# Kernel optimization log

Measured on AMD Instinct MI355X. Metric: run time of the kernel, lower is better.

## Reference

```python
import jax, jax.numpy as jnp
import numpy as np

B_, N_, E_, NNZ = 64, 1723, 1723, 16384
CIN, COUT = 256, 256
H1, H2, H3 = 64, 32, 128  # lin1 out, HGCN hidden, HGCN out (hidden_channels=128)


def layernorm(x, g, b, eps=1e-5):
    mu = jnp.mean(x, axis=-1, keepdims=True)
    var = jnp.mean((x - mu) ** 2, axis=-1, keepdims=True)
    return (x - mu) * jax.lax.rsqrt(var + eps) * g + b


def graph_linear(x, W, b):
    # x: (B, Cin, N) -> (B, Cout, N), matches torch.matmul(W[None], x) + b[None,:,None]
    return jnp.einsum('oc,bcn->bon', W, x) + b[None, :, None]


def hconv(x, node_idx, edge_idx, theta, bias):
    # PyG HypergraphConv (no attention): X' = D^-1 H W B^-1 H^T X Theta + bias
    x = jnp.einsum('bnc,oc->bno', x, theta)  # lin (bias=False)
    ones = jnp.ones(node_idx.shape, x.dtype)
    Dd = jax.ops.segment_sum(ones, node_idx, num_segments=N_)  # node degree
    Bd = jax.ops.segment_sum(ones, edge_idx, num_segments=E_)  # hyperedge degree
    Dinv = jnp.where(Dd > 0, 1.0 / Dd, 0.0)
    Binv = jnp.where(Bd > 0, 1.0 / Bd, 0.0)
    # node -> hyperedge aggregation, message scaled by B^-1 of target edge
    msg = jnp.swapaxes(x[:, node_idx, :] * Binv[edge_idx][None, :, None], 0, 1)  # (nnz,B,C)
    ef = jax.ops.segment_sum(msg, edge_idx, num_segments=E_)  # (E,B,C)
    # hyperedge -> node aggregation, message scaled by D^-1 of target node
    msg2 = ef[edge_idx] * Dinv[node_idx][:, None, None]  # (nnz,B,C)
    out = jax.ops.segment_sum(msg2, node_idx, num_segments=N_)  # (N,B,C)
    return jnp.swapaxes(out, 0, 1) + bias


def setup_inputs():
    key = jax.random.key(0)
    ks = jax.random.split(key, 8)
    s = 0.02
    return {
        'x': jax.random.normal(ks[0], (B_, N_, CIN), jnp.float32),
        'incident_matrix': jax.random.randint(ks[1], (2, NNZ), 0, N_, jnp.int32),
        'pre_g': jnp.ones((CIN,), jnp.float32),
        'pre_b': jnp.zeros((CIN,), jnp.float32),
        'lin1_W': jax.random.normal(ks[2], (H1, CIN), jnp.float32) * s,
        'lin1_b': jnp.zeros((H1,), jnp.float32),
        'n1_g': jnp.ones((H1,), jnp.float32),
        'n1_b': jnp.zeros((H1,), jnp.float32),
        'th1': jax.random.normal(ks[3], (H2, H1), jnp.float32) * s,
        'bi1': jnp.zeros((H2,), jnp.float32),
        'th2': jax.random.normal(ks[4], (H3, H2), jnp.float32) * s,
        'bi2': jnp.zeros((H3,), jnp.float32),
        'n2_g': jnp.ones((H3,), jnp.float32),
        'n2_b': jnp.zeros((H3,), jnp.float32),
        'lin2_W': jax.random.normal(ks[5], (COUT, H3), jnp.float32) * s,
        'lin2_b': jnp.zeros((COUT,), jnp.float32),
    }


def reference(x, incident_matrix, pre_g, pre_b, lin1_W, lin1_b, n1_g, n1_b,
              th1, bi1, th2, bi2, n2_g, n2_b, lin2_W, lin2_b):
    node_idx, edge_idx = incident_matrix[0], incident_matrix[1]
    ty = jnp.swapaxes(jax.nn.relu(layernorm(x, pre_g, pre_b)), 1, 2)  # (B,Cin,N)
    y = jnp.swapaxes(graph_linear(ty, lin1_W, lin1_b), 1, 2)          # (B,N,64)
    y = jax.nn.relu(layernorm(y, n1_g, n1_b))
    y = hconv(y, node_idx, edge_idx, th1, bi1)                         # (B,N,32)
    y = hconv(y, node_idx, edge_idx, th2, bi2)                         # (B,N,128)
    ty = jnp.swapaxes(jax.nn.relu(layernorm(y, n2_g, n2_b)), 1, 2)
    y = jnp.swapaxes(graph_linear(ty, lin2_W, lin2_b), 1, 2)           # (B,N,256)
    return x + y  # skip_conv declared in module but unused in forward
```

## Files before the change

kernel.cpp:

```cpp
#include <hip/hip_runtime.h>
#include <cstdint>

constexpr int B  = 64;
constexpr int N  = 1723;
constexpr int E  = 1723;
constexpr int NNZ = 16384;
constexpr int ROWS = B * N;

typedef __bf16 bf16x8 __attribute__((ext_vector_type(8)));
typedef float  f32x4  __attribute__((ext_vector_type(4)));

constexpr size_t OFF_DD   = 0;
constexpr size_t OFF_BD   = OFF_DD + E;
constexpr size_t OFF_NCUR = OFF_BD + E;
constexpr size_t OFF_ECUR = OFF_NCUR + E;
constexpr size_t OFF_NOFF = OFF_ECUR + E;
constexpr size_t OFF_EOFF = OFF_NOFF + (E + 1);
constexpr size_t OFF_NVAL = OFF_EOFF + (E + 1);
constexpr size_t OFF_EVAL = OFF_NVAL + NNZ;

constexpr int WB_LIN1 = 0;
constexpr int WB_TH1  = 16384;
constexpr int WB_TH2  = 18432;
constexpr int WB_LIN2 = 22528;
constexpr int WB_TOT  = 55296;
constexpr int CVT_BLOCKS  = WB_TOT / 8 / 256;
constexpr int ZERO_INTS   = 4 * E;
constexpr int ZERO_BLOCKS = (ZERO_INTS + 255) / 256;

constexpr size_t B_WB    = 262144;
constexpr size_t B_SLOTA = 1u << 20;
constexpr size_t B_SLOTB = B_SLOTA + (30u << 20);
constexpr size_t B_SLOTC = B_SLOTB + (8u << 20);
constexpr size_t B_SLOTD = B_SLOTC + (8u << 20);

__device__ __forceinline__ ushort f2bf(float f) {
  uint32_t b = __float_as_uint(f);
  b += 0x7fffu + ((b >> 16) & 1u);
  return (ushort)(b >> 16);
}
__device__ __forceinline__ float bf2f(ushort u) {
  return __uint_as_float((uint32_t)u << 16);
}
union U16x8 { uint4 q; ushort s[8]; };

__global__ __launch_bounds__(256) void k_init(const float* __restrict__ W1, const float* __restrict__ W2,
                                              const float* __restrict__ W3, const float* __restrict__ W4,
                                              ushort* __restrict__ out, int* __restrict__ zr) {
  int bid = blockIdx.x;
  if (bid < CVT_BLOCKS) {
    int e = (bid * 256 + threadIdx.x) * 8;
    const float* src;
    int off;
    if (e < WB_TH1)      { src = W1; off = e - WB_LIN1; }
    else if (e < WB_TH2) { src = W2; off = e - WB_TH1; }
    else if (e < WB_LIN2){ src = W3; off = e - WB_TH2; }
    else                 { src = W4; off = e - WB_LIN2; }
    float4 v0 = *(const float4*)(src + off);
    float4 v1 = *(const float4*)(src + off + 4);
    U16x8 u;
    u.s[0] = f2bf(v0.x); u.s[1] = f2bf(v0.y); u.s[2] = f2bf(v0.z); u.s[3] = f2bf(v0.w);
    u.s[4] = f2bf(v1.x); u.s[5] = f2bf(v1.y); u.s[6] = f2bf(v1.z); u.s[7] = f2bf(v1.w);
    *(uint4*)(out + e) = u.q;
  } else {
    int i = (bid - CVT_BLOCKS) * 256 + threadIdx.x;
    if (i < ZERO_INTS) zr[i] = 0;
  }
}

__global__ __launch_bounds__(256) void k_hist(const int* __restrict__ inc,
                                              int* __restrict__ Dd, int* __restrict__ Bd) {
  int k = blockIdx.x * 256 + threadIdx.x;
  atomicAdd(&Dd[inc[k]], 1);
  atomicAdd(&Bd[inc[NNZ + k]], 1);
}

__global__ __launch_bounds__(256) void k_scan(const int* __restrict__ Dd, const int* __restrict__ Bd,
                                              int* __restrict__ noff, int* __restrict__ eoff) {
  __shared__ int part[256];
  const int t = threadIdx.x;
  for (int pass = 0; pass < 2; ++pass) {
    const int* cnt = pass ? Bd : Dd;
    int* off = pass ? eoff : noff;
    constexpr int CH = 7;
    int loc[CH];
    int s = 0;
    int base = t * CH;
#pragma unroll
    for (int i = 0; i < CH; ++i) {
      int idx = base + i;
      loc[i] = (idx < E) ? cnt[idx] : 0;
      s += loc[i];
    }
    part[t] = s;
    __syncthreads();
    for (int d = 1; d < 256; d <<= 1) {
      int v = (t >= d) ? part[t - d] : 0;
      __syncthreads();
      part[t] += v;
      __syncthreads();
    }
    int pre = (t > 0) ? part[t - 1] : 0;
#pragma unroll
    for (int i = 0; i < CH; ++i) {
      int idx = base + i;
      if (idx < E) off[idx] = pre;
      pre += loc[i];
    }
    if (t == 255) off[E] = pre;
    __syncthreads();
  }
}

__global__ __launch_bounds__(256) void k_fill(const int* __restrict__ inc,
                                              const int* __restrict__ noff, const int* __restrict__ eoff,
                                              int* __restrict__ ncur, int* __restrict__ ecur,
                                              int* __restrict__ nval, int* __restrict__ eval) {
  int k = blockIdx.x * 256 + threadIdx.x;
  int n = inc[k], e = inc[NNZ + k];
  int p = atomicAdd(&ecur[e], 1);
  eval[eoff[e] + p] = n;
  int q = atomicAdd(&ncur[n], 1);
  nval[noff[n] + q] = e;
}

__global__ __launch_bounds__(256) void k_sort2(const int* __restrict__ noff, int* __restrict__ nval,
                                               const int* __restrict__ eoff, int* __restrict__ eval) {
  __shared__ int buf[256][33];
  int s = blockIdx.x * 256 + threadIdx.x;
  const int* off;
  int* vals;
  if (s < E) { off = noff; vals = nval; }
  else if (s < 2 * E) { off = eoff; vals = eval; s -= E; }
  else return;
  int b = off[s], e = off[s + 1], len = e - b;
  int* loc = buf[threadIdx.x];
  if (len <= 32) {
    for (int i = 0; i < len; ++i) loc[i] = vals[b + i];
    for (int i = 1; i < len; ++i) {
      int v = loc[i];
      int j = i - 1;
      while (j >= 0 && loc[j] > v) { loc[j + 1] = loc[j]; --j; }
      loc[j + 1] = v;
    }
    for (int i = 0; i < len; ++i) vals[b + i] = loc[i];
  } else {
    for (int i = b + 1; i < e; ++i) {
      int v = vals[i];
      int j = i - 1;
      while (j >= b && vals[j] > v) { vals[j + 1] = vals[j]; --j; }
      vals[j + 1] = v;
    }
  }
}

__global__ __launch_bounds__(256, 3) void k_lin1th1(const float* __restrict__ x,
                                                    const ushort* __restrict__ Wb,
                                                    const float* __restrict__ lin1_b,
                                                    const float* __restrict__ pre_g,
                                                    const float* __restrict__ pre_b,
                                                    const float* __restrict__ n1_g,
                                                    const float* __restrict__ n1_b,
                                                    ushort* __restrict__ xl1) {
  __shared__ __align__(16) uint4 R0[2048];
  __shared__ __align__(16) uint4 W2s[256];
  __shared__ float2 st[64];

  const int t = threadIdx.x;
  const int r0 = blockIdx.x * 64;
  const ushort* W1 = Wb + WB_LIN1;
  const ushort* W2 = Wb + WB_TH1;

  const int lane = t & 63;
  const int w = t >> 6;
  const int lo = lane & 15, hi = lane >> 4;
  const int wm = w & 1, wn = w >> 1;
  const int m0 = wm * 32 + lo, m1 = wm * 32 + 16 + lo;

  bf16x8 wf[16];
#pragma unroll
  for (int ks = 0; ks < 8; ++ks)
#pragma unroll
    for (int f = 0; f < 2; ++f) {
      int n = wn * 32 + f * 16 + lo;
      wf[ks * 2 + f] = *(const bf16x8*)(W1 + (size_t)n * 256 + (ks * 4 + hi) * 8);
    }

  {
    int row = t >> 3, c = t & 7;
    W2s[row * 8 + (c ^ (row & 7))] = *(const uint4*)(W2 + row * 64 + c * 8);
  }
#pragma unroll
  for (int i = 0; i < 8; ++i) {
    int idx = t + i * 256;
    int row = idx >> 5, c = idx & 31;
    const float* src = x + (size_t)(r0 + row) * 256 + c * 8;
    float4 v0 = *(const float4*)src;
    float4 v1 = *(const float4*)(src + 4);
    U16x8 u;
    u.s[0] = f2bf(v0.x); u.s[1] = f2bf(v0.y); u.s[2] = f2bf(v0.z); u.s[3] = f2bf(v0.w);
    u.s[4] = f2bf(v1.x); u.s[5] = f2bf(v1.y); u.s[6] = f2bf(v1.z); u.s[7] = f2bf(v1.w);
    R0[row * 32 + (c ^ (row & 7))] = u.q;
  }
  __syncthreads();

  {
    int row = t >> 2, part = t & 3;
    float s1 = 0.f, s2 = 0.f;
#pragma unroll
    for (int i = 0; i < 8; ++i) {
      int c = part * 8 + i;
      U16x8 u; u.q = R0[row * 32 + (c ^ (row & 7))];
#pragma unroll
      for (int j = 0; j < 8; ++j) { float v = bf2f(u.s[j]); s1 += v; s2 += v * v; }
    }
    s1 += __shfl_xor(s1, 1, 64); s2 += __shfl_xor(s2, 1, 64);
    s1 += __shfl_xor(s1, 2, 64); s2 += __shfl_xor(s2, 2, 64);
    if (part == 0) {
      float mu = s1 / 256.f;
      float var = fmaxf(s2 / 256.f - mu * mu, 0.f);
      st[row] = make_float2(mu, rsqrtf(var + 1e-5f));
    }
  }
  __syncthreads();
#pragma unroll
  for (int i = 0; i < 8; ++i) {
    int idx = t + i * 256;
    int row = idx >> 5, c = idx & 31;
    int slot = row * 32 + (c ^ (row & 7));
    U16x8 u; u.q = R0[slot];
    float2 s = st[row];
    float4 g0 = *(const float4*)(pre_g + c * 8);
    float4 g1 = *(const float4*)(pre_g + c * 8 + 4);
    float4 b0 = *(const float4*)(pre_b + c * 8);
    float4 b1 = *(const float4*)(pre_b + c * 8 + 4);
    U16x8 o;
    o.s[0] = f2bf(fmaxf(fmaf((bf2f(u.s[0]) - s.x) * s.y, g0.x, b0.x), 0.f));
    o.s[1] = f2bf(fmaxf(fmaf((bf2f(u.s[1]) - s.x) * s.y, g0.y, b0.y), 0.f));
    o.s[2] = f2bf(fmaxf(fmaf((bf2f(u.s[2]) - s.x) * s.y, g0.z, b0.z), 0.f));
    o.s[3] = f2bf(fmaxf(fmaf((bf2f(u.s[3]) - s.x) * s.y, g0.w, b0.w), 0.f));
    o.s[4] = f2bf(fmaxf(fmaf((bf2f(u.s[4]) - s.x) * s.y, g1.x, b1.x), 0.f));
    o.s[5] = f2bf(fmaxf(fmaf((bf2f(u.s[5]) - s.x) * s.y, g1.y, b1.y), 0.f));
    o.s[6] = f2bf(fmaxf(fmaf((bf2f(u.s[6]) - s.x) * s.y, g1.z, b1.z), 0.f));
    o.s[7] = f2bf(fmaxf(fmaf((bf2f(u.s[7]) - s.x) * s.y, g1.w, b1.w), 0.f));
    R0[slot] = o.q;
  }
  __syncthreads();

  const bf16x8* Asv = (const bf16x8*)R0;
  f32x4 acc1[2][2] = {};
#pragma unroll
  for (int ks = 0; ks < 8; ++ks) {
    int cb = ks * 4 + hi;
    bf16x8 a0 = Asv[m0 * 32 + (cb ^ (m0 & 7))];
    bf16x8 a1 = Asv[m1 * 32 + (cb ^ (m1 & 7))];
#pragma unroll
    for (int f = 0; f < 2; ++f) {
      acc1[0][f] = __builtin_amdgcn_mfma_f32_16x16x32_bf16(a0, wf[ks * 2 + f], acc1[0][f], 0, 0, 0);
      acc1[1][f] = __builtin_amdgcn_mfma_f32_16x16x32_bf16(a1, wf[ks * 2 + f], acc1[1][f], 0, 0, 0);
    }
  }
  __syncthreads();

  float* ost = (float*)R0;
#pragma unroll
  for (int f = 0; f < 2; ++f) {
    int colg = wn * 32 + f * 16 + lo;
    float badd = lin1_b[colg];
#pragma unroll
    for (int i = 0; i < 2; ++i)
#pragma unroll
      for (int r = 0; r < 4; ++r) {
        int lr = wm * 32 + i * 16 + hi * 4 + r;
        ost[lr * 68 + colg] = acc1[i][f][r] + badd;
      }
  }
  __syncthreads();

  {
    int row = t >> 2, part = t & 3;
    float s1 = 0.f, s2 = 0.f;
#pragma unroll
    for (int i = 0; i < 16; ++i) {
      float v = ost[row * 68 + part * 16 + i];
      s1 += v; s2 += v * v;
    }
    s1 += __shfl_xor(s1, 1, 64); s2 += __shfl_xor(s2, 1, 64);
    s1 += __shfl_xor(s1, 2, 64); s2 += __shfl_xor(s2, 2, 64);
    if (part == 0) {
      float mu = s1 / 64.f;
      float var = fmaxf(s2 / 64.f - mu * mu, 0.f);
      st[row] = make_float2(mu, rsqrtf(var + 1e-5f));
    }
  }
  __syncthreads();
  uint4* A2q = R0 + 1152;
#pragma unroll
  for (int i = 0; i < 2; ++i) {
    int idx = t + i * 256;
    int row = idx >> 3, c = idx & 7;
    float2 s = st[row];
    U16x8 u;
#pragma unroll
    for (int j = 0; j < 8; ++j) {
      int col = c * 8 + j;
      float v = ost[row * 68 + col];
      u.s[j] = f2bf(fmaxf(fmaf((v - s.x) * s.y, n1_g[col], n1_b[col]), 0.f));
    }
    A2q[row * 8 + (c ^ (row & 7))] = u.q;
  }
  __syncthreads();

  const bf16x8* A2v = (const bf16x8*)A2q;
  f32x4 acc2[2] = {};
#pragma unroll
  for (int ks = 0; ks < 2; ++ks) {
    int cb = ks * 4 + hi;
    bf16x8 a0 = A2v[m0 * 8 + (cb ^ (m0 & 7))];
    bf16x8 a1 = A2v[m1 * 8 + (cb ^ (m1 & 7))];
    int n = wn * 16 + lo;
    bf16x8 bfr = ((const bf16x8*)W2s)[n * 8 + (cb ^ (n & 7))];
    acc2[0] = __builtin_amdgcn_mfma_f32_16x16x32_bf16(a0, bfr, acc2[0], 0, 0, 0);
    acc2[1] = __builtin_amdgcn_mfma_f32_16x16x32_bf16(a1, bfr, acc2[1], 0, 0, 0);
  }
  {
    int colg = wn * 16 + lo;
#pragma unroll
    for (int i = 0; i < 2; ++i)
#pragma unroll
      for (int r = 0; r < 4; ++r) {
        int lr = wm * 32 + i * 16 + hi * 4 + r;
        ost[lr * 36 + colg] = acc2[i][r];
      }
  }
  __syncthreads();
  {
    int lr = t >> 2, c8 = t & 3;
    uint32_t r = r0 + lr;
    uint32_t b_ = r / (uint32_t)N;
    uint32_t n_ = r - b_ * (uint32_t)N;
    U16x8 u;
#pragma unroll
    for (int j = 0; j < 8; ++j) u.s[j] = f2bf(ost[lr * 36 + c8 * 8 + j]);
    *(uint4*)(xl1 + ((size_t)n_ * 64 + b_) * 32 + c8 * 8) = u.q;
  }
}

template <bool HASB>
__global__ __launch_bounds__(256) void agg_bf16_k(const ushort* __restrict__ in,
                                                  const int* __restrict__ off,
                                                  const int* __restrict__ vals,
                                                  const float* __restrict__ bias,
                                                  ushort* __restrict__ outb) {
  const int seg = blockIdx.x;
  const int beg = off[seg], end = off[seg + 1];
  const int t = threadIdx.x;
  float acc[8] = {0.f, 0.f, 0.f, 0.f, 0.f, 0.f, 0.f, 0.f};
  if (beg < end) {
    uint4 cur = *(const uint4*)(in + (size_t)vals[beg] * 2048 + t * 8);
    for (int k = beg + 1; k < end; ++k) {
      uint4 nxt = *(const uint4*)(in + (size_t)vals[k] * 2048 + t * 8);
      U16x8 u; u.q = cur;
#pragma unroll
      for (int j = 0; j < 8; ++j) acc[j] += bf2f(u.s[j]);
      cur = nxt;
    }
    U16x8 u; u.q = cur;
#pragma unroll
    for (int j = 0; j < 8; ++j) acc[j] += bf2f(u.s[j]);
  }
  float inv = (end > beg) ? 1.f / (float)(end - beg) : 0.f;
  U16x8 o;
  if constexpr (HASB) {
    int cb = (t & 3) * 8;
#pragma unroll
    for (int j = 0; j < 8; ++j) o.s[j] = f2bf(acc[j] * inv + bias[cb + j]);
  } else {
#pragma unroll
    for (int j = 0; j < 8; ++j) o.s[j] = f2bf(acc[j] * inv);
  }
  *(uint4*)(outb + (size_t)seg * 2048 + t * 8) = o.q;
}

__global__ __launch_bounds__(256, 2) void k_aggth2(const ushort* __restrict__ ef2,
                                                   const int* __restrict__ noff,
                                                   const int* __restrict__ nval,
                                                   const ushort* __restrict__ W2b,
                                                   const float* __restrict__ bi2,
                                                   const float* __restrict__ n2_g,
                                                   const float* __restrict__ n2_b,
                                                   ushort* __restrict__ y3n) {
  __shared__ __align__(16) uint4 A2s[256];
  __shared__ __align__(16) uint4 W2s[512];
  __shared__ float ost[64 * 132];
  __shared__ float2 st[64];
  const int t = threadIdx.x;
  const int seg = blockIdx.x;

#pragma unroll
  for (int i = 0; i < 2; ++i) {
    int idx = t + i * 256;
    int row = idx >> 2, c = idx & 3;
    W2s[row * 4 + (c ^ (row & 3))] = *(const uint4*)(W2b + row * 32 + c * 8);
  }
  const int beg = noff[seg], end = noff[seg + 1];
  float acc[8] = {0.f, 0.f, 0.f, 0.f, 0.f, 0.f, 0.f, 0.f};
  if (beg < end) {
    uint4 cur = *(const uint4*)(ef2 + (size_t)nval[beg] * 2048 + t * 8);
    for (int k = beg + 1; k < end; ++k) {
      uint4 nxt = *(const uint4*)(ef2 + (size_t)nval[k] * 2048 + t * 8);
      U16x8 u; u.q = cur;
#pragma unroll
      for (int j = 0; j < 8; ++j) acc[j] += bf2f(u.s[j]);
      cur = nxt;
    }
    U16x8 u; u.q = cur;
#pragma unroll
    for (int j = 0; j < 8; ++j) acc[j] += bf2f(u.s[j]);
  }
  float inv = (end > beg) ? 1.f / (float)(end - beg) : 0.f;
  {
    U16x8 u;
#pragma unroll
    for (int j = 0; j < 8; ++j) u.s[j] = f2bf(acc[j] * inv);
    int row = t >> 2, c = t & 3;
    A2s[row * 4 + (c ^ (row & 3))] = u.q;
  }
  __syncthreads();

  const int lane = t & 63;
  const int w = t >> 6;
  const int lo = lane & 15, hi = lane >> 4;
  const int wm = w & 1, wn = w >> 1;
  const int m0 = wm * 32 + lo, m1 = wm * 32 + 16 + lo;
  const bf16x8* Asv = (const bf16x8*)A2s;
  const bf16x8* Wsv = (const bf16x8*)W2s;
  f32x4 acc2[2][4] = {};
  {
    bf16x8 a0 = Asv[m0 * 4 + (hi ^ (m0 & 3))];
    bf16x8 a1 = Asv[m1 * 4 + (hi ^ (m1 & 3))];
#pragma unroll
    for (int f = 0; f < 4; ++f) {
      int n = wn * 64 + f * 16 + lo;
      bf16x8 bfr = Wsv[n * 4 + (hi ^ (n & 3))];
      acc2[0][f] = __builtin_amdgcn_mfma_f32_16x16x32_bf16(a0, bfr, acc2[0][f], 0, 0, 0);
      acc2[1][f] = __builtin_amdgcn_mfma_f32_16x16x32_bf16(a1, bfr, acc2[1][f], 0, 0, 0);
    }
  }
#pragma unroll
  for (int f = 0; f < 4; ++f) {
    int colg = wn * 64 + f * 16 + lo;
    float badd = bi2[colg];
#pragma unroll
    for (int i = 0; i < 2; ++i)
#pragma unroll
      for (int r = 0; r < 4; ++r) {
        int lr = wm * 32 + i * 16 + hi * 4 + r;
        ost[lr * 132 + colg] = acc2[i][f][r] + badd;
      }
  }
  __syncthreads();
  {
    int row = t >> 2, part = t & 3;
    float s1 = 0.f, s2 = 0.f;
#pragma unroll
    for (int i = 0; i < 32; ++i) {
      float v = ost[row * 132 + part * 32 + i];
      s1 += v; s2 += v * v;
    }
    s1 += __shfl_xor(s1, 1, 64); s2 += __shfl_xor(s2, 1, 64);
    s1 += __shfl_xor(s1, 2, 64); s2 += __shfl_xor(s2, 2, 64);
    if (part == 0) {
      float mu = s1 / 128.f;
      float var = fmaxf(s2 / 128.f - mu * mu, 0.f);
      st[row] = make_float2(mu, rsqrtf(var + 1e-5f));
    }
  }
  __syncthreads();
#pragma unroll
  for (int i = 0; i < 4; ++i) {
    int idx = t + i * 256;
    int row = idx >> 4, c = idx & 15;
    float2 s = st[row];
    U16x8 u;
#pragma unroll
    for (int j = 0; j < 8; ++j) {
      int col = c * 8 + j;
      float v = ost[row * 132 + col];
      u.s[j] = f2bf(fmaxf(fmaf((v - s.x) * s.y, n2_g[col], n2_b[col]), 0.f));
    }
    *(uint4*)(y3n + ((size_t)seg * 64 + row) * 128 + c * 8) = u.q;
  }
}

constexpr int NWG2 = (ROWS / 64) * 4;
__global__ __launch_bounds__(256, 2) void k_lin2(const ushort* __restrict__ y3n,
                                                 const ushort* __restrict__ Wl2,
                                                 const float* __restrict__ lin2_b,
                                                 const float* __restrict__ x,
                                                 float* __restrict__ out) {
  __shared__ __align__(16) uint4 smem[2048];
  const int t = threadIdx.x;
  int orig = blockIdx.x;
  int xcd = orig & 7;
  int idx0 = orig >> 3;
  constexpr int q = NWG2 / 8, r = NWG2 % 8;
  int wgid = (xcd < r ? xcd * (q + 1) : r * (q + 1) + (xcd - r) * q) + idx0;
  const int tile = wgid & 3;
  const int r0 = (wgid >> 2) * 64;
  const int c0 = tile * 64;
  uint4* AsQ = smem;
  uint4* WsQ = smem + 1024;

#pragma unroll
  for (int i = 0; i < 4; ++i) {
    int idx = t + i * 256;
    int row = idx >> 4, c = idx & 15;
    AsQ[row * 16 + (c ^ (row & 7))] = *(const uint4*)(y3n + (size_t)(r0 + row) * 128 + c * 8);
  }
#pragma unroll
  for (int i = 0; i < 4; ++i) {
    int idx = t + i * 256;
    int row = idx >> 4, c = idx & 15;
    WsQ[row * 16 + (c ^ (row & 7))] = *(const uint4*)(Wl2 + (size_t)(c0 + row) * 128 + c * 8);
  }
  __syncthreads();

  const int lane = t & 63;
  const int w = t >> 6;
  const int lo = lane & 15, hi = lane >> 4;
  const int wm = w & 1, wn = w >> 1;
  const int m0 = wm * 32 + lo, m1 = wm * 32 + 16 + lo;
  const bf16x8* Asv = (const bf16x8*)AsQ;
  const bf16x8* Wsv = (const bf16x8*)WsQ;
  f32x4 acc[2][2] = {};
#pragma unroll
  for (int ks = 0; ks < 4; ++ks) {
    int cb = ks * 4 + hi;
    bf16x8 a0 = Asv[m0 * 16 + (cb ^ (m0 & 7))];
    bf16x8 a1 = Asv[m1 * 16 + (cb ^ (m1 & 7))];
#pragma unroll
    for (int f = 0; f < 2; ++f) {
      int n = wn * 32 + f * 16 + lo;
      bf16x8 bfr = Wsv[n * 16 + (cb ^ (n & 7))];
      acc[0][f] = __builtin_amdgcn_mfma_f32_16x16x32_bf16(a0, bfr, acc[0][f], 0, 0, 0);
      acc[1][f] = __builtin_amdgcn_mfma_f32_16x16x32_bf16(a1, bfr, acc[1][f], 0, 0, 0);
    }
  }
  __syncthreads();

  float* ost = (float*)smem;
#pragma unroll
  for (int f = 0; f < 2; ++f) {
    int cl = wn * 32 + f * 16 + lo;
    float badd = lin2_b[c0 + cl];
#pragma unroll
    for (int i = 0; i < 2; ++i)
#pragma unroll
      for (int r2 = 0; r2 < 4; ++r2) {
        int lr = wm * 32 + i * 16 + hi * 4 + r2;
        ost[lr * 68 + cl] = acc[i][f][r2] + badd;
      }
  }
  __syncthreads();

#pragma unroll
  for (int i = 0; i < 4; ++i) {
    int idx = t + i * 256;
    int lr = idx >> 4, c4 = idx & 15;
    uint32_t rr = r0 + lr;
    uint32_t n_ = rr >> 6, b_ = rr & 63u;
    size_t obase = ((size_t)b_ * N + n_) * 256 + c0 + c4 * 4;
    float4 v = *(const float4*)&ost[lr * 68 + c4 * 4];
    float4 s = *(const float4*)(x + obase);
    v.x += s.x; v.y += s.y; v.z += s.z; v.w += s.w;
    *(float4*)(out + obase) = v;
  }
}

extern "C" void kernel_launch(void* const* d_in, const int* in_sizes, int n_in,
                              void* d_out, int out_size, void* d_ws, size_t ws_size,
                              hipStream_t stream) {
  const float* x      = (const float*)d_in[0];
  const int*   inc    = (const int*)  d_in[1];
  const float* pre_g  = (const float*)d_in[2];
  const float* pre_b  = (const float*)d_in[3];
  const float* lin1_W = (const float*)d_in[4];
  const float* lin1_b = (const float*)d_in[5];
  const float* n1_g   = (const float*)d_in[6];
  const float* n1_b   = (const float*)d_in[7];
  const float* th1    = (const float*)d_in[8];
  const float* bi1    = (const float*)d_in[9];
  const float* th2    = (const float*)d_in[10];
  const float* bi2    = (const float*)d_in[11];
  const float* n2_g   = (const float*)d_in[12];
  const float* n2_b   = (const float*)d_in[13];
  const float* lin2_W = (const float*)d_in[14];
  const float* lin2_b = (const float*)d_in[15];
  float* out = (float*)d_out;
  char* ws = (char*)d_ws;

  int* meta = (int*)ws;
  int* Dd   = meta + OFF_DD;
  int* Bd   = meta + OFF_BD;
  int* ncur = meta + OFF_NCUR;
  int* ecur = meta + OFF_ECUR;
  int* noff = meta + OFF_NOFF;
  int* eoff = meta + OFF_EOFF;
  int* nval = meta + OFF_NVAL;
  int* eval = meta + OFF_EVAL;

  ushort* Wbase = (ushort*)(ws + B_WB);
  ushort* y3n = (ushort*)(ws + B_SLOTA);
  ushort* xl1 = (ushort*)(ws + B_SLOTB);
  ushort* ef2 = (ushort*)(ws + B_SLOTB);
  ushort* ef1 = (ushort*)(ws + B_SLOTC);
  ushort* y2  = (ushort*)(ws + B_SLOTD);

  k_init<<<CVT_BLOCKS + ZERO_BLOCKS, 256, 0, stream>>>(lin1_W, th1, th2, lin2_W, Wbase, meta);

  k_hist<<<NNZ / 256, 256, 0, stream>>>(inc, Dd, Bd);
  k_scan<<<1, 256, 0, stream>>>(Dd, Bd, noff, eoff);
  k_fill<<<NNZ / 256, 256, 0, stream>>>(inc, noff, eoff, ncur, ecur, nval, eval);
  k_sort2<<<(2 * E + 255) / 256, 256, 0, stream>>>(noff, nval, eoff, eval);

  k_lin1th1<<<ROWS / 64, 256, 0, stream>>>(x, Wbase, lin1_b, pre_g, pre_b, n1_g, n1_b, xl1);

  agg_bf16_k<false><<<E, 256, 0, stream>>>(xl1, eoff, eval, nullptr, ef1);
  agg_bf16_k<true ><<<E, 256, 0, stream>>>(ef1, noff, nval, bi1, y2);
  agg_bf16_k<false><<<E, 256, 0, stream>>>(y2, eoff, eval, nullptr, ef2);

  k_aggth2<<<E, 256, 0, stream>>>(ef2, noff, nval, Wbase + WB_TH2, bi2, n2_g, n2_b, y3n);

  k_lin2<<<NWG2, 256, 0, stream>>>(y3n, Wbase + WB_LIN2, lin2_b, x, out);
}
```

Measured before the change: 165.9 us.

## Fuse final aggregation, theta2, layernorm with lin2 and residual into one kernel

Merges the k_aggth2 and k_lin2 kernels so that each node's 64x128 normalized activations stay in shared memory and feed the lin2 MFMA directly. The full lin2 weight (256x128) is loaded in two halves per block, and the output plus residual is written per node across the batch. This removes the y3n round trip through global memory and one launch. In exchange, each block re-reads the whole lin2 weight, uses more LDS (which may limit occupancy), and writes rows strided by N, giving less coalesced output.

```diff
diff --git a/kernel.cpp b/kernel.cpp
--- a/kernel.cpp
+++ b/kernel.cpp
@@ -29,8 +29,7 @@
 constexpr int ZERO_BLOCKS = (ZERO_INTS + 255) / 256;
 
 constexpr size_t B_WB    = 262144;
-constexpr size_t B_SLOTA = 1u << 20;
-constexpr size_t B_SLOTB = B_SLOTA + (30u << 20);
+constexpr size_t B_SLOTB = 4u << 20;
 constexpr size_t B_SLOTC = B_SLOTB + (8u << 20);
 constexpr size_t B_SLOTD = B_SLOTC + (8u << 20);
 
@@ -382,20 +381,30 @@
   *(uint4*)(outb + (size_t)seg * 2048 + t * 8) = o.q;
 }
 
-__global__ __launch_bounds__(256, 2) void k_aggth2(const ushort* __restrict__ ef2,
-                                                   const int* __restrict__ noff,
-                                                   const int* __restrict__ nval,
-                                                   const ushort* __restrict__ W2b,
-                                                   const float* __restrict__ bi2,
-                                                   const float* __restrict__ n2_g,
-                                                   const float* __restrict__ n2_b,
-                                                   ushort* __restrict__ y3n) {
+__global__ __launch_bounds__(256, 2) void k_aggl2(const ushort* __restrict__ ef2,
+                                                  const int* __restrict__ noff,
+                                                  const int* __restrict__ nval,
+                                                  const ushort* __restrict__ W2b,
+                                                  const float* __restrict__ bi2,
+                                                  const float* __restrict__ n2_g,
+                                                  const float* __restrict__ n2_b,
+                                                  const ushort* __restrict__ Wl2,
+                                                  const float* __restrict__ lin2_b,
+                                                  const float* __restrict__ x,
+                                                  float* __restrict__ out) {
   __shared__ __align__(16) uint4 A2s[256];
   __shared__ __align__(16) uint4 W2s[512];
-  __shared__ float ost[64 * 132];
+  __shared__ __align__(16) uint4 AsQ[1024];
+  __shared__ __align__(16) char  big[34816];
   __shared__ float2 st[64];
   const int t = threadIdx.x;
   const int seg = blockIdx.x;
+
+  const int lane = t & 63;
+  const int w = t >> 6;
+  const int lo = lane & 15, hi = lane >> 4;
+  const int wm = w & 1, wn = w >> 1;
+  const int m0 = wm * 32 + lo, m1 = wm * 32 + 16 + lo;
 
 #pragma unroll
   for (int i = 0; i < 2; ++i) {
@@ -428,15 +437,11 @@
   }
   __syncthreads();
 
-  const int lane = t & 63;
-  const int w = t >> 6;
-  const int lo = lane & 15, hi = lane >> 4;
-  const int wm = w & 1, wn = w >> 1;
-  const int m0 = wm * 32 + lo, m1 = wm * 32 + 16 + lo;
-  const bf16x8* Asv = (const bf16x8*)A2s;
-  const bf16x8* Wsv = (const bf16x8*)W2s;
-  f32x4 acc2[2][4] = {};
-  {
+  float* ost = (float*)big;
+  {
+    const bf16x8* Asv = (const bf16x8*)A2s;
+    const bf16x8* Wsv = (const bf16x8*)W2s;
+    f32x4 acc2[2][4] = {};
     bf16x8 a0 = Asv[m0 * 4 + (hi ^ (m0 & 3))];
     bf16x8 a1 = Asv[m1 * 4 + (hi ^ (m1 & 3))];
 #pragma unroll
@@ -446,18 +451,18 @@
       acc2[0][f] = __builtin_amdgcn_mfma_f32_16x16x32_bf16(a0, bfr, acc2[0][f], 0, 0, 0);
       acc2[1][f] = __builtin_amdgcn_mfma_f32_16x16x32_bf16(a1, bfr, acc2[1][f], 0, 0, 0);
     }
-  }
-#pragma unroll
-  for (int f = 0; f < 4; ++f) {
-    int colg = wn * 64 + f * 16 + lo;
-    float badd = bi2[colg];
-#pragma unroll
-    for (int i = 0; i < 2; ++i)
-#pragma unroll
-      for (int r = 0; r < 4; ++r) {
-        int lr = wm * 32 + i * 16 + hi * 4 + r;
-        ost[lr * 132 + colg] = acc2[i][f][r] + badd;
-      }
+#pragma unroll
+    for (int f = 0; f < 4; ++f) {
+      int colg = wn * 64 + f * 16 + lo;
+      float badd = bi2[colg];
+#pragma unroll
+      for (int i = 0; i < 2; ++i)
+#pragma unroll
+        for (int r = 0; r < 4; ++r) {
+          int lr = wm * 32 + i * 16 + hi * 4 + r;
+          ost[lr * 132 + colg] = acc2[i][f][r] + badd;
+        }
+    }
   }
   __syncthreads();
   {
@@ -489,92 +494,67 @@
       float v = ost[row * 132 + col];
       u.s[j] = f2bf(fmaxf(fmaf((v - s.x) * s.y, n2_g[col], n2_b[col]), 0.f));
     }
-    *(uint4*)(y3n + ((size_t)seg * 64 + row) * 128 + c * 8) = u.q;
-  }
-}
-
-constexpr int NWG2 = (ROWS / 64) * 4;
-__global__ __launch_bounds__(256, 2) void k_lin2(const ushort* __restrict__ y3n,
-                                                 const ushort* __restrict__ Wl2,
-                                                 const float* __restrict__ lin2_b,
-                                                 const float* __restrict__ x,
-                                                 float* __restrict__ out) {
-  __shared__ __align__(16) uint4 smem[2048];
-  const int t = threadIdx.x;
-  int orig = blockIdx.x;
-  int xcd = orig & 7;
-  int idx0 = orig >> 3;
-  constexpr int q = NWG2 / 8, r = NWG2 % 8;
-  int wgid = (xcd < r ? xcd * (q + 1) : r * (q + 1) + (xcd - r) * q) + idx0;
-  const int tile = wgid & 3;
-  const int r0 = (wgid >> 2) * 64;
-  const int c0 = tile * 64;
-  uint4* AsQ = smem;
-  uint4* WsQ = smem + 1024;
-
-#pragma unroll
-  for (int i = 0; i < 4; ++i) {
-    int idx = t + i * 256;
-    int row = idx >> 4, c = idx & 15;
-    AsQ[row * 16 + (c ^ (row & 7))] = *(const uint4*)(y3n + (size_t)(r0 + row) * 128 + c * 8);
-  }
-#pragma unroll
-  for (int i = 0; i < 4; ++i) {
-    int idx = t + i * 256;
-    int row = idx >> 4, c = idx & 15;
-    WsQ[row * 16 + (c ^ (row & 7))] = *(const uint4*)(Wl2 + (size_t)(c0 + row) * 128 + c * 8);
-  }
-  __syncthreads();
-
-  const int lane = t & 63;
-  const int w = t >> 6;
-  const int lo = lane & 15, hi = lane >> 4;
-  const int wm = w & 1, wn = w >> 1;
-  const int m0 = wm * 32 + lo, m1 = wm * 32 + 16 + lo;
+    AsQ[row * 16 + (c ^ (row & 7))] = u.q;
+  }
+  __syncthreads();
+
   const bf16x8* Asv = (const bf16x8*)AsQ;
-  const bf16x8* Wsv = (const bf16x8*)WsQ;
-  f32x4 acc[2][2] = {};
-#pragma unroll
-  for (int ks = 0; ks < 4; ++ks) {
-    int cb = ks * 4 + hi;
-    bf16x8 a0 = Asv[m0 * 16 + (cb ^ (m0 & 7))];
-    bf16x8 a1 = Asv[m1 * 16 + (cb ^ (m1 & 7))];
-#pragma unroll
-    for (int f = 0; f < 2; ++f) {
-      int n = wn * 32 + f * 16 + lo;
-      bf16x8 bfr = Wsv[n * 16 + (cb ^ (n & 7))];
-      acc[0][f] = __builtin_amdgcn_mfma_f32_16x16x32_bf16(a0, bfr, acc[0][f], 0, 0, 0);
-      acc[1][f] = __builtin_amdgcn_mfma_f32_16x16x32_bf16(a1, bfr, acc[1][f], 0, 0, 0);
-    }
-  }
-  __syncthreads();
-
-  float* ost = (float*)smem;
-#pragma unroll
-  for (int f = 0; f < 2; ++f) {
-    int cl = wn * 32 + f * 16 + lo;
-    float badd = lin2_b[c0 + cl];
-#pragma unroll
-    for (int i = 0; i < 2; ++i)
-#pragma unroll
-      for (int r2 = 0; r2 < 4; ++r2) {
-        int lr = wm * 32 + i * 16 + hi * 4 + r2;
-        ost[lr * 68 + cl] = acc[i][f][r2] + badd;
+  uint4* WsQ = (uint4*)big;
+#pragma unroll
+  for (int half = 0; half < 2; ++half) {
+#pragma unroll
+    for (int i = 0; i < 8; ++i) {
+      int idx = t + i * 256;
+      int row = idx >> 4, c = idx & 15;
+      WsQ[row * 16 + (c ^ (row & 7))] = *(const uint4*)(Wl2 + (size_t)(half * 128 + row) * 128 + c * 8);
+    }
+    __syncthreads();
+    const bf16x8* Wsv = (const bf16x8*)WsQ;
+    f32x4 accl[2][4] = {};
+#pragma unroll
+    for (int ks = 0; ks < 4; ++ks) {
+      int cb = ks * 4 + hi;
+      bf16x8 a0 = Asv[m0 * 16 + (cb ^ (m0 & 7))];
+      bf16x8 a1 = Asv[m1 * 16 + (cb ^ (m1 & 7))];
+#pragma unroll
+      for (int f = 0; f < 4; ++f) {
+        int n = wn * 64 + f * 16 + lo;
+        bf16x8 bfr = Wsv[n * 16 + (cb ^ (n & 7))];
+        accl[0][f] = __builtin_amdgcn_mfma_f32_16x16x32_bf16(a0, bfr, accl[0][f], 0, 0, 0);
+        accl[1][f] = __builtin_amdgcn_mfma_f32_16x16x32_bf16(a1, bfr, accl[1][f], 0, 0, 0);
       }
-  }
-  __syncthreads();
-
-#pragma unroll
-  for (int i = 0; i < 4; ++i) {
-    int idx = t + i * 256;
-    int lr = idx >> 4, c4 = idx & 15;
-    uint32_t rr = r0 + lr;
-    uint32_t n_ = rr >> 6, b_ = rr & 63u;
-    size_t obase = ((size_t)b_ * N + n_) * 256 + c0 + c4 * 4;
-    float4 v = *(const float4*)&ost[lr * 68 + c4 * 4];
-    float4 s = *(const float4*)(x + obase);
-    v.x += s.x; v.y += s.y; v.z += s.z; v.w += s.w;
-    *(float4*)(out + obase) = v;
+    }
+    __syncthreads();
+    float* epi = (float*)big;
+#pragma unroll
+    for (int chunk = 0; chunk < 2; ++chunk) {
+      if (wn == chunk) {
+#pragma unroll
+        for (int f = 0; f < 4; ++f) {
+          int cl = f * 16 + lo;
+          float badd = lin2_b[half * 128 + chunk * 64 + cl];
+#pragma unroll
+          for (int i = 0; i < 2; ++i)
+#pragma unroll
+            for (int r = 0; r < 4; ++r) {
+              int lr = wm * 32 + i * 16 + hi * 4 + r;
+              epi[lr * 68 + cl] = accl[i][f][r] + badd;
+            }
+        }
+      }
+      __syncthreads();
+#pragma unroll
+      for (int i = 0; i < 4; ++i) {
+        int idx = t + i * 256;
+        int lr = idx >> 4, c4 = idx & 15;
+        size_t obase = ((size_t)lr * N + seg) * 256 + half * 128 + chunk * 64 + c4 * 4;
+        float4 v = *(const float4*)&epi[lr * 68 + c4 * 4];
+        float4 s = *(const float4*)(x + obase);
+        v.x += s.x; v.y += s.y; v.z += s.z; v.w += s.w;
+        *(float4*)(out + obase) = v;
+      }
+      __syncthreads();
+    }
   }
 }
 
@@ -611,14 +591,12 @@
   int* eval = meta + OFF_EVAL;
 
   ushort* Wbase = (ushort*)(ws + B_WB);
-  ushort* y3n = (ushort*)(ws + B_SLOTA);
   ushort* xl1 = (ushort*)(ws + B_SLOTB);
   ushort* ef2 = (ushort*)(ws + B_SLOTB);
   ushort* ef1 = (ushort*)(ws + B_SLOTC);
   ushort* y2  = (ushort*)(ws + B_SLOTD);
 
   k_init<<<CVT_BLOCKS + ZERO_BLOCKS, 256, 0, stream>>>(lin1_W, th1, th2, lin2_W, Wbase, meta);
-
   k_hist<<<NNZ / 256, 256, 0, stream>>>(inc, Dd, Bd);
   k_scan<<<1, 256, 0, stream>>>(Dd, Bd, noff, eoff);
   k_fill<<<NNZ / 256, 256, 0, stream>>>(inc, noff, eoff, ncur, ecur, nval, eval);
@@ -630,7 +608,6 @@
   agg_bf16_k<true ><<<E, 256, 0, stream>>>(ef1, noff, nval, bi1, y2);
   agg_bf16_k<false><<<E, 256, 0, stream>>>(y2, eoff, eval, nullptr, ef2);
 
-  k_aggth2<<<E, 256, 0, stream>>>(ef2, noff, nval, Wbase + WB_TH2, bi2, n2_g, n2_b, y3n);
-
-  k_lin2<<<NWG2, 256, 0, stream>>>(y3n, Wbase + WB_LIN2, lin2_b, x, out);
-}
+  k_aggl2<<<E, 256, 0, stream>>>(ef2, noff, nval, Wbase + WB_TH2, bi2, n2_g, n2_b,
+                                 Wbase + WB_LIN2, lin2_b, x, out);
+}
```

Result: slower. 172.8 us (+4.2%).
